# Optimization experiments

Hardware: AMD Instinct MI355X
Metric: run time of the kernel (lower is better)

## Reference

```python
import jax, jax.numpy as jnp
import numpy as np

H = W = 56; WS = 7; SHIFT = 3; HEADS = 4; DIM = 128
HD = DIM // HEADS; SCALE = HD ** -0.5
NW = (H // WS) * (W // WS)  # 64 windows per image
N = WS * WS                 # 49 tokens per window
HID = int(DIM * 4.0)


def _rel_index():
    coords = np.stack(np.meshgrid(np.arange(WS), np.arange(WS), indexing='ij'))  # (2,WS,WS)
    cf = coords.reshape(2, -1)
    rel = (cf[:, :, None] - cf[:, None, :]).transpose(1, 2, 0)  # (N,N,2)
    rel[:, :, 0] += WS - 1
    rel[:, :, 1] += WS - 1
    rel[:, :, 0] *= 2 * WS - 1
    return jnp.asarray(rel.sum(-1))  # (N,N) int indices into bias table


def _attn_mask():
    img = np.zeros((H, W))
    cnt = 0
    for hs in (slice(0, -WS), slice(-WS, -SHIFT), slice(-SHIFT, None)):
        for ws in (slice(0, -WS), slice(-WS, -SHIFT), slice(-SHIFT, None)):
            img[hs, ws] = cnt
            cnt += 1
    mw = img.reshape(H // WS, WS, W // WS, WS).transpose(0, 2, 1, 3).reshape(-1, N)
    diff = mw[:, None, :] - mw[:, :, None]
    return jnp.asarray(np.where(diff != 0, -100.0, 0.0).astype(np.float32))  # (NW,N,N)

REL_IDX = _rel_index()
ATTN_MASK = _attn_mask()


def _ln(x, g, b):
    m = jnp.mean(x, -1, keepdims=True)
    v = jnp.var(x, -1, keepdims=True)
    return (x - m) * jax.lax.rsqrt(v + 1e-5) * g + b


def _win_part(x):  # (B,H,W,C) -> (B*NW, N, C)
    B = x.shape[0]
    x = x.reshape(B, H // WS, WS, W // WS, WS, DIM)
    return x.transpose(0, 1, 3, 2, 4, 5).reshape(-1, N, DIM)


def _win_rev(x, B):  # (B*NW, N, C) -> (B,H,W,C)
    x = x.reshape(B, H // WS, W // WS, WS, WS, DIM)
    return x.transpose(0, 1, 3, 2, 4, 5).reshape(B, H, W, DIM)


def setup_inputs() -> dict:
    key = jax.random.key(0)
    ks = jax.random.split(key, 8)
    s = 0.02
    return {
        'x': jax.random.normal(ks[0], (64, H * W, DIM), jnp.float32),
        'g1': jnp.ones((DIM,), jnp.float32),
        'b1': jnp.zeros((DIM,), jnp.float32),
        'qkv_w': jax.random.normal(ks[1], (3 * DIM, DIM), jnp.float32) * s,
        'qkv_b': jnp.zeros((3 * DIM,), jnp.float32),
        'rpb_table': jax.random.normal(ks[2], ((2 * WS - 1) ** 2, HEADS), jnp.float32) * s,
        'proj_w': jax.random.normal(ks[3], (DIM, DIM), jnp.float32) * s,
        'proj_b': jnp.zeros((DIM,), jnp.float32),
        'g2': jnp.ones((DIM,), jnp.float32),
        'b2': jnp.zeros((DIM,), jnp.float32),
        'fc1_w': jax.random.normal(ks[4], (HID, DIM), jnp.float32) * s,
        'fc1_b': jnp.zeros((HID,), jnp.float32),
        'fc2_w': jax.random.normal(ks[5], (DIM, HID), jnp.float32) * s,
        'fc2_b': jnp.zeros((DIM,), jnp.float32),
    }


def reference(x, g1, b1, qkv_w, qkv_b, rpb_table, proj_w, proj_b, g2, b2, fc1_w, fc1_b, fc2_w, fc2_b):
    B = x.shape[0]
    shortcut = x
    h = _ln(x, g1, b1).reshape(B, H, W, DIM)
    # cyclic shift + window partition
    h = jnp.roll(h, shift=(-SHIFT, -SHIFT), axis=(1, 2))
    xw = _win_part(h)  # (B*NW, N, C)
    B_ = xw.shape[0]
    # window attention
    qkv = (xw @ qkv_w.T + qkv_b).reshape(B_, N, 3, HEADS, HD).transpose(2, 0, 3, 1, 4)
    q, k, v = qkv[0] * SCALE, qkv[1], qkv[2]  # (B_, heads, N, hd)
    attn = jnp.einsum('bhnd,bhmd->bhnm', q, k)
    bias = rpb_table[REL_IDX.reshape(-1)].reshape(N, N, HEADS).transpose(2, 0, 1)  # (heads,N,N)
    attn = attn + bias[None]
    attn = attn.reshape(B, NW, HEADS, N, N) + ATTN_MASK[None, :, None]
    attn = jax.nn.softmax(attn.reshape(B_, HEADS, N, N), axis=-1)
    out = jnp.einsum('bhnm,bhmd->bhnd', attn, v).transpose(0, 2, 1, 3).reshape(B_, N, DIM)
    out = out @ proj_w.T + proj_b
    # reverse windows + reverse shift
    h = _win_rev(out, B)
    h = jnp.roll(h, shift=(SHIFT, SHIFT), axis=(1, 2)).reshape(B, H * W, DIM)
    x = shortcut + h
    # MLP
    y = _ln(x, g2, b2)
    y = jax.nn.gelu(y @ fc1_w.T + fc1_b, approximate=False)
    y = y @ fc2_w.T + fc2_b
    return x + y
```

## Files before the change

### kernel.cpp

```cpp
#include <hip/hip_runtime.h>

typedef unsigned int uint;
typedef unsigned short ushort;
using short8 = __attribute__((ext_vector_type(8))) short;
using f32x4  = __attribute__((ext_vector_type(4))) float;
using uint4v = __attribute__((ext_vector_type(4))) uint;

#define SCALE_ 0.17677669529663687f
#define MFMA(a,b,c) __builtin_amdgcn_mfma_f32_16x16x32_bf16(a,b,c,0,0,0)

__device__ inline ushort f2bf(float f){
  uint u = __float_as_uint(f);
  return (ushort)((u + 0x7fffu + ((u >> 16) & 1u)) >> 16);
}
__device__ inline uint pk2(float a, float b){
  return (uint)f2bf(a) | ((uint)f2bf(b) << 16);
}
__device__ inline float gelu(float v){
  return 0.5f * v * (1.f + erff(v * 0.70710678f));
}

__global__ __launch_bounds__(256) void prep_kernel(
    const float* __restrict__ qkv_w, const float* __restrict__ qkv_b,
    const float* __restrict__ rpb, const float* __restrict__ proj_w,
    const float* __restrict__ fc1_w, const float* __restrict__ fc2_w,
    ushort* __restrict__ qkv_wb, float* __restrict__ qkv_bs,
    ushort* __restrict__ proj_wb, ushort* __restrict__ fc1_wb,
    ushort* __restrict__ fc2_wb, float* __restrict__ T2)
{
  int i = blockIdx.x * 256 + threadIdx.x;
  if (i < 49152) qkv_wb[i] = f2bf(qkv_w[i] * (i < 16384 ? SCALE_ : 1.f));
  if (i < 16384) proj_wb[i] = f2bf(proj_w[i]);
  if (i < 65536) { fc1_wb[i] = f2bf(fc1_w[i]); fc2_wb[i] = f2bf(fc2_w[i]); }
  if (i < 384)   qkv_bs[i] = qkv_b[i] * (i < 128 ? SCALE_ : 1.f);
  if (i < 65536) {
    int cls = i >> 14, h = (i >> 12) & 3, tok = (i >> 6) & 63, key = i & 63;
    float val = -30000.f;
    if (tok < 49 && key < 49) {
      int ri = tok / 7, ci = tok - ri * 7, rj = key / 7, cj = key - rj * 7;
      val = rpb[((ri - rj + 6) * 13 + (ci - cj + 6)) * 4 + h];
      int er = cls >> 1, ec = cls & 1;
      int regi = (er ? (ri < 4 ? 1 : 2) : 0) * 3 + (ec ? (ci < 4 ? 1 : 2) : 0);
      int regj = (er ? (rj < 4 ? 1 : 2) : 0) * 3 + (ec ? (cj < 4 ? 1 : 2) : 0);
      if (regi != regj) val -= 100.f;
    }
    T2[i] = val;
  }
}

__global__ __launch_bounds__(256, 3) void attn_kernel(
    const float* __restrict__ x, const float* __restrict__ g1, const float* __restrict__ b1,
    const ushort* __restrict__ qkv_wb, const float* __restrict__ qkv_bs,
    const float* __restrict__ T2, const ushort* __restrict__ proj_wb,
    const float* __restrict__ proj_b, float* __restrict__ x_new)
{
  __shared__ __align__(16) char smem[49152];
  const int tid = threadIdx.x;
  const int w = tid >> 6, lane = tid & 63;
  const int g = lane >> 4, li = lane & 15;
  const int blk = blockIdx.x;
  const int b = blk >> 6, wi = blk & 63;
  const int wr = wi >> 3, wc = wi & 7;
  const float* xb = x + (size_t)b * (3136 * 128);
  char* qls = smem + w * 4096;
  char* kls = smem + 16384 + w * 4096;
  char* vls = smem + 32768 + w * 4096;
  char* xls = smem + 32768;
  ushort* oa = (ushort*)smem;
  float* Rp = (float*)(smem + 17408);
  const f32x4 zf = {0.f, 0.f, 0.f, 0.f};

#pragma unroll
  for (int it = 0; it < 7; ++it) {
    int gi = it * 256 + tid;
    bool ok = gi < 1568;
    int t = ok ? (gi >> 5) : 48;
    int ch4 = (gi & 31) << 2;
    int tr = t / 7, tc = t - tr * 7;
    int rr = wr * 7 + tr + 3; rr -= (rr >= 56) ? 56 : 0;
    int cc = wc * 7 + tc + 3; cc -= (cc >= 56) ? 56 : 0;
    float4 v = *(const float4*)(xb + (size_t)(rr * 56 + cc) * 128 + ch4);
    float s = v.x + v.y + v.z + v.w;
    float s2 = v.x*v.x + v.y*v.y + v.z*v.z + v.w*v.w;
#pragma unroll
    for (int off = 16; off; off >>= 1) { s += __shfl_xor(s, off); s2 += __shfl_xor(s2, off); }
    float mn = s * 0.0078125f;
    float rs = rsqrtf(s2 * 0.0078125f - mn * mn + 1e-5f);
    if (ok) {
      float4 gg = *(const float4*)(g1 + ch4);
      float4 bb = *(const float4*)(b1 + ch4);
      uint2 u;
      u.x = pk2((v.x - mn) * rs * gg.x + bb.x, (v.y - mn) * rs * gg.y + bb.y);
      u.y = pk2((v.z - mn) * rs * gg.z + bb.z, (v.w - mn) * rs * gg.w + bb.w);
      int slot = ch4 >> 3;
      int tokx = t ^ ((slot & 7) << 1);
      *(uint2*)(xls + (slot * 64 + tokx) * 16 + ((ch4 & 4) << 1)) = u;
    }
  }
  if (tid < 240) {
    int slot = tid & 15, t = 49 + (tid >> 4);
    int tokx = t ^ ((slot & 7) << 1);
    uint4 z = make_uint4(0u, 0u, 0u, 0u);
    *(uint4*)(xls + (slot * 64 + tokx) * 16) = z;
  }
  __syncthreads();

  f32x4 qacc[2][4], kacc[2][4], vacc[4][2];
#pragma unroll
  for (int cf = 0; cf < 2; ++cf)
#pragma unroll
    for (int m = 0; m < 4; ++m) { qacc[cf][m] = zf; kacc[cf][m] = zf; vacc[m][cf] = zf; }

#pragma unroll
  for (int kt = 0; kt < 4; ++kt) {
    const int slot = kt * 4 + g;
    short8 xf[4];
#pragma unroll
    for (int m = 0; m < 4; ++m)
      xf[m] = *(const short8*)(xls + (slot * 64 + ((m * 16 + li) ^ ((slot & 7) << 1))) * 16);
    const int wofs = kt * 32 + g * 8;
#pragma unroll
    for (int cf = 0; cf < 2; ++cf) {
      short8 wq = *(const short8*)(qkv_wb + (size_t)(w * 32 + cf * 16 + li) * 128 + wofs);
#pragma unroll
      for (int m = 0; m < 4; ++m) qacc[cf][m] = MFMA(wq, xf[m], qacc[cf][m]);
    }
#pragma unroll
    for (int cf = 0; cf < 2; ++cf) {
      short8 wk = *(const short8*)(qkv_wb + (size_t)(128 + w * 32 + cf * 16 + li) * 128 + wofs);
#pragma unroll
      for (int m = 0; m < 4; ++m) kacc[cf][m] = MFMA(wk, xf[m], kacc[cf][m]);
    }
#pragma unroll
    for (int cf = 0; cf < 2; ++cf) {
      short8 wv = *(const short8*)(qkv_wb + (size_t)(256 + w * 32 + cf * 16 + li) * 128 + wofs);
#pragma unroll
      for (int m = 0; m < 4; ++m) vacc[m][cf] = MFMA(xf[m], wv, vacc[m][cf]);
    }
  }
#pragma unroll
  for (int cf = 0; cf < 2; ++cf) {
    f32x4 qb4 = *(const f32x4*)(qkv_bs + w * 32 + cf * 16 + g * 4);
    f32x4 kb4 = *(const f32x4*)(qkv_bs + 128 + w * 32 + cf * 16 + g * 4);
    const int qkoff = (cf * 2 + (g >> 1)) * 1024 + (g & 1) * 8;
#pragma unroll
    for (int m = 0; m < 4; ++m) {
      f32x4 qv = qacc[cf][m] + qb4;
      uint2 qu; qu.x = pk2(qv[0], qv[1]); qu.y = pk2(qv[2], qv[3]);
      *(uint2*)(qls + qkoff + (m * 16 + li) * 16) = qu;
      f32x4 kv = kacc[cf][m] + kb4;
      uint2 ku; ku.x = pk2(kv[0], kv[1]); ku.y = pk2(kv[2], kv[3]);
      *(uint2*)(kls + qkoff + (m * 16 + li) * 16) = ku;
    }
  }
  __syncthreads();
#pragma unroll
  for (int cf = 0; cf < 2; ++cf) {
    float vb = qkv_bs[256 + w * 32 + cf * 16 + li];
#pragma unroll
    for (int m = 0; m < 4; ++m) {
      f32x4 vv = vacc[m][cf];
      uint2 vu; vu.x = pk2(vv[0] + vb, vv[1] + vb); vu.y = pk2(vv[2] + vb, vv[3] + vb);
      *(uint2*)(vls + (m * 2 + (g >> 1)) * 1024 + (cf * 16 + li) * 16 + (g & 1) * 8) = vu;
    }
  }

  f32x4 oacc[2][4];
  {
    const int cls = ((wr == 7) ? 2 : 0) | ((wc == 7) ? 1 : 0);
    const float* Tb = T2 + ((cls * 4 + w) << 12);
    short8 kf[4];
#pragma unroll
    for (int n = 0; n < 4; ++n)
      kf[n] = *(const short8*)(kls + g * 1024 + (n * 16 + li) * 16);
    uint up[4][4][2];
#pragma unroll
    for (int m = 0; m < 4; ++m) {
      short8 qf = *(const short8*)(qls + g * 1024 + (m * 16 + li) * 16);
      f32x4 s[4];
#pragma unroll
      for (int n = 0; n < 4; ++n) {
        s[n] = MFMA(kf[n], qf, zf);
        s[n] += *(const f32x4*)(Tb + (m * 16 + li) * 64 + n * 16 + g * 4);
      }
      float mx = -3.4e38f;
#pragma unroll
      for (int n = 0; n < 4; ++n)
        mx = fmaxf(mx, fmaxf(fmaxf(s[n][0], s[n][1]), fmaxf(s[n][2], s[n][3])));
      mx = fmaxf(mx, __shfl_xor(mx, 16));
      mx = fmaxf(mx, __shfl_xor(mx, 32));
      float sum = 0.f;
#pragma unroll
      for (int n = 0; n < 4; ++n)
#pragma unroll
        for (int r = 0; r < 4; ++r) { float e = __expf(s[n][r] - mx); s[n][r] = e; sum += e; }
      sum += __shfl_xor(sum, 16); sum += __shfl_xor(sum, 32);
      float rsm = 1.f / sum;
#pragma unroll
      for (int n = 0; n < 4; ++n) {
        up[m][n][0] = pk2(s[n][0] * rsm, s[n][1] * rsm);
        up[m][n][1] = pk2(s[n][2] * rsm, s[n][3] * rsm);
      }
    }
#pragma unroll
    for (int cf = 0; cf < 2; ++cf)
#pragma unroll
      for (int m = 0; m < 4; ++m) oacc[cf][m] = zf;
    const int srcA = ((g & 1) << 5) + li;
    const int hi = g >> 1;
#pragma unroll
    for (int kt = 0; kt < 2; ++kt) {
      short8 vt0 = *(const short8*)(vls + (kt * 4 + g) * 1024 + li * 16);
      short8 vt1 = *(const short8*)(vls + (kt * 4 + g) * 1024 + (16 + li) * 16);
#pragma unroll
      for (int m = 0; m < 4; ++m) {
        uint t00 = __shfl(up[m][kt * 2][0], srcA),      t10 = __shfl(up[m][kt * 2 + 1][0], srcA);
        uint t01 = __shfl(up[m][kt * 2][1], srcA),      t11 = __shfl(up[m][kt * 2 + 1][1], srcA);
        uint t02 = __shfl(up[m][kt * 2][0], srcA + 16), t12 = __shfl(up[m][kt * 2 + 1][0], srcA + 16);
        uint t03 = __shfl(up[m][kt * 2][1], srcA + 16), t13 = __shfl(up[m][kt * 2 + 1][1], srcA + 16);
        uint4v pu = { hi ? t10 : t00, hi ? t11 : t01, hi ? t12 : t02, hi ? t13 : t03 };
        short8 pf = __builtin_bit_cast(short8, pu);
        oacc[0][m] = MFMA(vt0, pf, oacc[0][m]);
        oacc[1][m] = MFMA(vt1, pf, oacc[1][m]);
      }
    }
  }
  __syncthreads();
#pragma unroll
  for (int cf = 0; cf < 2; ++cf)
#pragma unroll
    for (int m = 0; m < 4; ++m) {
      uint2 ou; ou.x = pk2(oacc[cf][m][0], oacc[cf][m][1]);
      ou.y = pk2(oacc[cf][m][2], oacc[cf][m][3]);
      *(uint2*)((char*)oa + ((m * 16 + li) * 136 + w * 32 + cf * 16 + g * 4) * 2) = ou;
    }
  __syncthreads();

  {
    f32x4 pacc[2][4];
#pragma unroll
    for (int cf = 0; cf < 2; ++cf)
#pragma unroll
      for (int m = 0; m < 4; ++m) pacc[cf][m] = zf;
#pragma unroll
    for (int kt = 0; kt < 4; ++kt) {
      short8 af[4];
#pragma unroll
      for (int m = 0; m < 4; ++m)
        af[m] = *(const short8*)((char*)oa + (m * 16 + li) * 272 + kt * 64 + g * 16);
#pragma unroll
      for (int cf = 0; cf < 2; ++cf) {
        short8 wp = *(const short8*)(proj_wb + (size_t)(w * 32 + cf * 16 + li) * 128 + kt * 32 + g * 8);
#pragma unroll
        for (int m = 0; m < 4; ++m) pacc[cf][m] = MFMA(af[m], wp, pacc[cf][m]);
      }
    }
#pragma unroll
    for (int cf = 0; cf < 2; ++cf) {
      int col = w * 32 + cf * 16 + li;
      float pb = proj_b[col];
#pragma unroll
      for (int m = 0; m < 4; ++m)
#pragma unroll
        for (int r = 0; r < 4; ++r) {
          int t2 = m * 16 + g * 4 + r;
          if (t2 < 49)
            Rp[t2 * 128 + (col ^ ((t2 & 7) << 2))] = pacc[cf][m][r] + pb;
        }
    }
  }
  __syncthreads();

#pragma unroll
  for (int it = 0; it < 7; ++it) {
    int gi = it * 256 + tid;
    if (gi < 1568) {
      int t = gi >> 5, ch4 = (gi & 31) << 2;
      int tr = t / 7, tc = t - tr * 7;
      int rr = wr * 7 + tr + 3; rr -= (rr >= 56) ? 56 : 0;
      int cc = wc * 7 + tc + 3; cc -= (cc >= 56) ? 56 : 0;
      size_t off = ((size_t)b * 3136 + rr * 56 + cc) * 128 + ch4;
      f32x4 d = *(const f32x4*)&Rp[t * 128 + (ch4 ^ ((t & 7) << 2))];
      float4 xr = *(const float4*)(x + off);
      float4 ov;
      ov.x = xr.x + d[0]; ov.y = xr.y + d[1];
      ov.z = xr.z + d[2]; ov.w = xr.w + d[3];
      *(float4*)(x_new + off) = ov;
    }
  }
}

__global__ __launch_bounds__(256, 4) void mlp_kernel(
    float* __restrict__ xio,
    const float* __restrict__ g2, const float* __restrict__ b2,
    const ushort* __restrict__ w1, const float* __restrict__ fb1,
    const ushort* __restrict__ w2, const float* __restrict__ fb2)
{
  __shared__ __align__(16) char smem[32768];
  char* Axs = smem;
  char* hls = smem + 16384;
  float* Rp = (float*)smem;
  const int tid = threadIdx.x, lane = tid & 63, w = tid >> 6;
  const int g = lane >> 4, li = lane & 15;
  float* xw = xio + (size_t)blockIdx.x * 64 * 128;
  const f32x4 zf = {0.f, 0.f, 0.f, 0.f};

#pragma unroll
  for (int it = 0; it < 8; ++it) {
    int gi = it * 256 + tid;
    int row = gi >> 5, ch4 = (gi & 31) << 2;
    float4 v = *(const float4*)(xw + row * 128 + ch4);
    float s = v.x + v.y + v.z + v.w;
    float s2 = v.x*v.x + v.y*v.y + v.z*v.z + v.w*v.w;
#pragma unroll
    for (int off = 16; off; off >>= 1) { s += __shfl_xor(s, off); s2 += __shfl_xor(s2, off); }
    float mn = s * 0.0078125f;
    float rs = rsqrtf(s2 * 0.0078125f - mn * mn + 1e-5f);
    float4 gg = *(const float4*)(g2 + ch4);
    float4 bb = *(const float4*)(b2 + ch4);
    uint2 u;
    u.x = pk2((v.x - mn) * rs * gg.x + bb.x, (v.y - mn) * rs * gg.y + bb.y);
    u.y = pk2((v.z - mn) * rs * gg.z + bb.z, (v.w - mn) * rs * gg.w + bb.w);
    int slot = ch4 >> 3;
    int tokx = row ^ ((slot & 7) << 1);
    *(uint2*)(Axs + (slot * 64 + tokx) * 16 + ((ch4 & 4) << 1)) = u;
  }
  __syncthreads();

  f32x4 acc2[4][2];
#pragma unroll
  for (int mi = 0; mi < 4; ++mi) { acc2[mi][0] = zf; acc2[mi][1] = zf; }

  for (int ck = 0; ck < 4; ++ck) {
    f32x4 acc1[2][4];
#pragma unroll
    for (int oi = 0; oi < 2; ++oi)
#pragma unroll
      for (int mi = 0; mi < 4; ++mi) acc1[oi][mi] = zf;
#pragma unroll
    for (int kt = 0; kt < 4; ++kt) {
      const int slot = kt * 4 + g;
      short8 xf[4];
#pragma unroll
      for (int mi = 0; mi < 4; ++mi)
        xf[mi] = *(const short8*)(Axs + (slot * 64 + ((mi * 16 + li) ^ ((slot & 7) << 1))) * 16);
#pragma unroll
      for (int oi = 0; oi < 2; ++oi) {
        short8 wf = *(const short8*)(w1 + (size_t)(ck * 128 + w * 32 + oi * 16 + li) * 128 + kt * 32 + g * 8);
#pragma unroll
        for (int mi = 0; mi < 4; ++mi) acc1[oi][mi] = MFMA(wf, xf[mi], acc1[oi][mi]);
      }
    }
#pragma unroll
    for (int oi = 0; oi < 2; ++oi) {
      f32x4 b4 = *(const f32x4*)(fb1 + ck * 128 + w * 32 + oi * 16 + g * 4);
#pragma unroll
      for (int mi = 0; mi < 4; ++mi) {
        f32x4 h = acc1[oi][mi] + b4;
        uint2 u; u.x = pk2(gelu(h[0]), gelu(h[1])); u.y = pk2(gelu(h[2]), gelu(h[3]));
        *(uint2*)(hls + ((w * 4 + oi * 2 + (g >> 1)) * 64 + mi * 16 + li) * 16 + ((g & 1) << 3)) = u;
      }
    }
    __syncthreads();
#pragma unroll
    for (int kt = 0; kt < 4; ++kt) {
      short8 hf[4];
#pragma unroll
      for (int mi = 0; mi < 4; ++mi)
        hf[mi] = *(const short8*)(hls + ((kt * 4 + g) * 64 + mi * 16 + li) * 16);
#pragma unroll
      for (int bo = 0; bo < 2; ++bo) {
        short8 wf = *(const short8*)(w2 + (size_t)(w * 32 + bo * 16 + li) * 512 + ck * 128 + kt * 32 + g * 8);
#pragma unroll
        for (int mi = 0; mi < 4; ++mi) acc2[mi][bo] = MFMA(hf[mi], wf, acc2[mi][bo]);
      }
    }
    __syncthreads();
  }

#pragma unroll
  for (int mi = 0; mi < 4; ++mi)
#pragma unroll
    for (int bo = 0; bo < 2; ++bo) {
      int out = w * 32 + bo * 16 + li;
#pragma unroll
      for (int r = 0; r < 4; ++r) {
        int tok = mi * 16 + g * 4 + r;
        Rp[tok * 128 + (out ^ ((tok & 7) << 2))] = acc2[mi][bo][r];
      }
    }
  __syncthreads();
#pragma unroll
  for (int it = 0; it < 8; ++it) {
    int gi = it * 256 + tid;
    int row = gi >> 5, ch4 = (gi & 31) << 2;
    f32x4 d = *(const f32x4*)&Rp[row * 128 + (ch4 ^ ((row & 7) << 2))];
    float4 xr = *(const float4*)(xw + row * 128 + ch4);
    float4 bb = *(const float4*)(fb2 + ch4);
    float4 ov;
    ov.x = xr.x + d[0] + bb.x; ov.y = xr.y + d[1] + bb.y;
    ov.z = xr.z + d[2] + bb.z; ov.w = xr.w + d[3] + bb.w;
    *(float4*)(xw + row * 128 + ch4) = ov;
  }
}

extern "C" void kernel_launch(void* const* d_in, const int* in_sizes, int n_in,
                              void* d_out, int out_size, void* d_ws, size_t ws_size,
                              hipStream_t stream)
{
  const float* x      = (const float*)d_in[0];
  const float* g1     = (const float*)d_in[1];
  const float* b1     = (const float*)d_in[2];
  const float* qkv_w  = (const float*)d_in[3];
  const float* qkv_b  = (const float*)d_in[4];
  const float* rpb    = (const float*)d_in[5];
  const float* proj_w = (const float*)d_in[6];
  const float* proj_b = (const float*)d_in[7];
  const float* g2     = (const float*)d_in[8];
  const float* b2     = (const float*)d_in[9];
  const float* fc1_w  = (const float*)d_in[10];
  const float* fc1_b  = (const float*)d_in[11];
  const float* fc2_w  = (const float*)d_in[12];
  const float* fc2_b  = (const float*)d_in[13];

  char* ws = (char*)d_ws;
  float*  T2      = (float*)ws;
  ushort* qkv_wb  = (ushort*)(ws + 262144);
  ushort* proj_wb = (ushort*)(ws + 360448);
  ushort* fc1_wb  = (ushort*)(ws + 393216);
  ushort* fc2_wb  = (ushort*)(ws + 524288);
  float*  qkv_bs  = (float*)(ws + 655360);
  float* out = (float*)d_out;

  prep_kernel<<<256, 256, 0, stream>>>(qkv_w, qkv_b, rpb, proj_w, fc1_w, fc2_w,
                                       qkv_wb, qkv_bs, proj_wb, fc1_wb, fc2_wb, T2);
  attn_kernel<<<4096, 256, 0, stream>>>(x, g1, b1, qkv_wb, qkv_bs, T2,
                                        proj_wb, proj_b, out);
  mlp_kernel<<<3136, 256, 0, stream>>>(out, g2, b2, fc1_wb, fc1_b, fc2_wb, fc2_b);
}
```

Before: 356.9 us.

## Fuse window attention and MLP into a single per-window kernel

Merges the attention kernel and the MLP kernel so each block processes one shifted window end to end. The residual result stays in registers and LDS instead of being written to global memory and re-read. The MLP now runs on 49-token windows padded to 64 rows, wasting about a quarter of its MFMA work. The fused kernel also keeps the attention kernel's launch bounds and larger LDS footprint, which can lower occupancy for the MLP phase and raise register pressure.

```diff
diff --git a/kernel.cpp b/kernel.cpp
--- a/kernel.cpp
+++ b/kernel.cpp
@@ -48,11 +48,15 @@
   }
 }
 
-__global__ __launch_bounds__(256, 3) void attn_kernel(
+__global__ __launch_bounds__(256, 3) void fused_kernel(
     const float* __restrict__ x, const float* __restrict__ g1, const float* __restrict__ b1,
     const ushort* __restrict__ qkv_wb, const float* __restrict__ qkv_bs,
     const float* __restrict__ T2, const ushort* __restrict__ proj_wb,
-    const float* __restrict__ proj_b, float* __restrict__ x_new)
+    const float* __restrict__ proj_b,
+    const float* __restrict__ g2, const float* __restrict__ b2,
+    const ushort* __restrict__ w1, const float* __restrict__ fb1,
+    const ushort* __restrict__ w2, const float* __restrict__ fb2,
+    float* __restrict__ out)
 {
   __shared__ __align__(16) char smem[49152];
   const int tid = threadIdx.x;
@@ -68,6 +72,9 @@
   char* xls = smem + 32768;
   ushort* oa = (ushort*)smem;
   float* Rp = (float*)(smem + 17408);
+  char* Axs = smem;
+  char* hls = smem + 16384;
+  float* Rp2 = (float*)smem;
   const f32x4 zf = {0.f, 0.f, 0.f, 0.f};
 
 #pragma unroll
@@ -271,59 +278,39 @@
   }
   __syncthreads();
 
-#pragma unroll
-  for (int it = 0; it < 7; ++it) {
-    int gi = it * 256 + tid;
-    if (gi < 1568) {
-      int t = gi >> 5, ch4 = (gi & 31) << 2;
-      int tr = t / 7, tc = t - tr * 7;
-      int rr = wr * 7 + tr + 3; rr -= (rr >= 56) ? 56 : 0;
-      int cc = wc * 7 + tc + 3; cc -= (cc >= 56) ? 56 : 0;
-      size_t off = ((size_t)b * 3136 + rr * 56 + cc) * 128 + ch4;
-      f32x4 d = *(const f32x4*)&Rp[t * 128 + (ch4 ^ ((t & 7) << 2))];
-      float4 xr = *(const float4*)(x + off);
-      float4 ov;
-      ov.x = xr.x + d[0]; ov.y = xr.y + d[1];
-      ov.z = xr.z + d[2]; ov.w = xr.w + d[3];
-      *(float4*)(x_new + off) = ov;
-    }
-  }
-}
-
-__global__ __launch_bounds__(256, 4) void mlp_kernel(
-    float* __restrict__ xio,
-    const float* __restrict__ g2, const float* __restrict__ b2,
-    const ushort* __restrict__ w1, const float* __restrict__ fb1,
-    const ushort* __restrict__ w2, const float* __restrict__ fb2)
-{
-  __shared__ __align__(16) char smem[32768];
-  char* Axs = smem;
-  char* hls = smem + 16384;
-  float* Rp = (float*)smem;
-  const int tid = threadIdx.x, lane = tid & 63, w = tid >> 6;
-  const int g = lane >> 4, li = lane & 15;
-  float* xw = xio + (size_t)blockIdx.x * 64 * 128;
-  const f32x4 zf = {0.f, 0.f, 0.f, 0.f};
-
-#pragma unroll
-  for (int it = 0; it < 8; ++it) {
-    int gi = it * 256 + tid;
-    int row = gi >> 5, ch4 = (gi & 31) << 2;
-    float4 v = *(const float4*)(xw + row * 128 + ch4);
-    float s = v.x + v.y + v.z + v.w;
-    float s2 = v.x*v.x + v.y*v.y + v.z*v.z + v.w*v.w;
-#pragma unroll
-    for (int off = 16; off; off >>= 1) { s += __shfl_xor(s, off); s2 += __shfl_xor(s2, off); }
-    float mn = s * 0.0078125f;
-    float rs = rsqrtf(s2 * 0.0078125f - mn * mn + 1e-5f);
+  float4 xn[8];
+  {
+    const int ch4 = (lane & 31) << 2;
+    const int half = lane >> 5;
+    const int row0 = w * 16;
     float4 gg = *(const float4*)(g2 + ch4);
     float4 bb = *(const float4*)(b2 + ch4);
-    uint2 u;
-    u.x = pk2((v.x - mn) * rs * gg.x + bb.x, (v.y - mn) * rs * gg.y + bb.y);
-    u.y = pk2((v.z - mn) * rs * gg.z + bb.z, (v.w - mn) * rs * gg.w + bb.w);
-    int slot = ch4 >> 3;
-    int tokx = row ^ ((slot & 7) << 1);
-    *(uint2*)(Axs + (slot * 64 + tokx) * 16 + ((ch4 & 4) << 1)) = u;
+#pragma unroll
+    for (int it = 0; it < 8; ++it) {
+      int t = row0 + it * 2 + half;
+      float4 v = make_float4(0.f, 0.f, 0.f, 0.f);
+      if (t < 49) {
+        int tr = t / 7, tc = t - tr * 7;
+        int rr = wr * 7 + tr + 3; rr -= (rr >= 56) ? 56 : 0;
+        int cc = wc * 7 + tc + 3; cc -= (cc >= 56) ? 56 : 0;
+        float4 xr = *(const float4*)(xb + (size_t)(rr * 56 + cc) * 128 + ch4);
+        f32x4 d = *(const f32x4*)&Rp[t * 128 + (ch4 ^ ((t & 7) << 2))];
+        v.x = xr.x + d[0]; v.y = xr.y + d[1]; v.z = xr.z + d[2]; v.w = xr.w + d[3];
+      }
+      xn[it] = v;
+      float s = v.x + v.y + v.z + v.w;
+      float s2 = v.x*v.x + v.y*v.y + v.z*v.z + v.w*v.w;
+#pragma unroll
+      for (int off = 16; off; off >>= 1) { s += __shfl_xor(s, off); s2 += __shfl_xor(s2, off); }
+      float mn = s * 0.0078125f;
+      float rs = rsqrtf(s2 * 0.0078125f - mn * mn + 1e-5f);
+      uint2 u;
+      u.x = pk2((v.x - mn) * rs * gg.x + bb.x, (v.y - mn) * rs * gg.y + bb.y);
+      u.y = pk2((v.z - mn) * rs * gg.z + bb.z, (v.w - mn) * rs * gg.w + bb.w);
+      int slot = ch4 >> 3;
+      int tokx = t ^ ((slot & 7) << 1);
+      *(uint2*)(Axs + (slot * 64 + tokx) * 16 + ((ch4 & 4) << 1)) = u;
+    }
   }
   __syncthreads();
 
@@ -382,25 +369,35 @@
   for (int mi = 0; mi < 4; ++mi)
 #pragma unroll
     for (int bo = 0; bo < 2; ++bo) {
-      int out = w * 32 + bo * 16 + li;
+      int och = w * 32 + bo * 16 + li;
 #pragma unroll
       for (int r = 0; r < 4; ++r) {
         int tok = mi * 16 + g * 4 + r;
-        Rp[tok * 128 + (out ^ ((tok & 7) << 2))] = acc2[mi][bo][r];
-      }
-    }
-  __syncthreads();
-#pragma unroll
-  for (int it = 0; it < 8; ++it) {
-    int gi = it * 256 + tid;
-    int row = gi >> 5, ch4 = (gi & 31) << 2;
-    f32x4 d = *(const f32x4*)&Rp[row * 128 + (ch4 ^ ((row & 7) << 2))];
-    float4 xr = *(const float4*)(xw + row * 128 + ch4);
-    float4 bb = *(const float4*)(fb2 + ch4);
-    float4 ov;
-    ov.x = xr.x + d[0] + bb.x; ov.y = xr.y + d[1] + bb.y;
-    ov.z = xr.z + d[2] + bb.z; ov.w = xr.w + d[3] + bb.w;
-    *(float4*)(xw + row * 128 + ch4) = ov;
+        Rp2[tok * 128 + (och ^ ((tok & 7) << 2))] = acc2[mi][bo][r];
+      }
+    }
+  __syncthreads();
+  {
+    const int ch4 = (lane & 31) << 2;
+    const int half = lane >> 5;
+    const int row0 = w * 16;
+    float4 fb4 = *(const float4*)(fb2 + ch4);
+    float* ob = out + (size_t)b * (3136 * 128);
+#pragma unroll
+    for (int it = 0; it < 8; ++it) {
+      int t = row0 + it * 2 + half;
+      if (t < 49) {
+        int tr = t / 7, tc = t - tr * 7;
+        int rr = wr * 7 + tr + 3; rr -= (rr >= 56) ? 56 : 0;
+        int cc = wc * 7 + tc + 3; cc -= (cc >= 56) ? 56 : 0;
+        f32x4 d = *(const f32x4*)&Rp2[t * 128 + (ch4 ^ ((t & 7) << 2))];
+        float4 v = xn[it];
+        float4 ov;
+        ov.x = v.x + d[0] + fb4.x; ov.y = v.y + d[1] + fb4.y;
+        ov.z = v.z + d[2] + fb4.z; ov.w = v.w + d[3] + fb4.w;
+        *(float4*)(ob + (size_t)(rr * 56 + cc) * 128 + ch4) = ov;
+      }
+    }
   }
 }
 
@@ -434,7 +431,7 @@
 
   prep_kernel<<<256, 256, 0, stream>>>(qkv_w, qkv_b, rpb, proj_w, fc1_w, fc2_w,
                                        qkv_wb, qkv_bs, proj_wb, fc1_wb, fc2_wb, T2);
-  attn_kernel<<<4096, 256, 0, stream>>>(x, g1, b1, qkv_wb, qkv_bs, T2,
-                                        proj_wb, proj_b, out);
-  mlp_kernel<<<3136, 256, 0, stream>>>(out, g2, b2, fc1_wb, fc1_b, fc2_wb, fc2_b);
-}
+  fused_kernel<<<4096, 256, 0, stream>>>(x, g1, b1, qkv_wb, qkv_bs, T2,
+                                         proj_wb, proj_b, g2, b2,
+                                         fc1_wb, fc1_b, fc2_wb, fc2_b, out);
+}
```

After: 468.4 us. 31.3% more time.

## Keep Q/K/V in registers via lane shuffles, shrink LDS for more occupancy

Applied to the files above, without the earlier changes.

Q, K and V are now computed one after another, packed to bf16 and kept in registers. Operand fragments for the QK^T and PV MFMAs are rebuilt with cross-lane shuffles instead of being staged through LDS, which removes the QKV LDS buffers and one barrier. Shared memory drops from 48KB to about 25KB, with the x, attention-output and projection buffers aliased on one region (an extra barrier guards the reuse), and launch bounds rise to 4 blocks per CU. The cost is many more shuffle instructions and higher register pressure under the tighter launch bound, which may cause spills.

```diff
diff --git a/kernel.cpp b/kernel.cpp
--- a/kernel.cpp
+++ b/kernel.cpp
@@ -48,13 +48,16 @@
   }
 }
 
-__global__ __launch_bounds__(256, 3) void attn_kernel(
+__global__ __launch_bounds__(256, 4) void attn_kernel(
     const float* __restrict__ x, const float* __restrict__ g1, const float* __restrict__ b1,
     const ushort* __restrict__ qkv_wb, const float* __restrict__ qkv_bs,
     const float* __restrict__ T2, const ushort* __restrict__ proj_wb,
     const float* __restrict__ proj_b, float* __restrict__ x_new)
 {
-  __shared__ __align__(16) char smem[49152];
+  __shared__ __align__(16) char smem[25088];
+  char*   xls = smem;
+  ushort* oa  = (ushort*)smem;
+  float*  Rp  = (float*)smem;
   const int tid = threadIdx.x;
   const int w = tid >> 6, lane = tid & 63;
   const int g = lane >> 4, li = lane & 15;
@@ -62,12 +65,6 @@
   const int b = blk >> 6, wi = blk & 63;
   const int wr = wi >> 3, wc = wi & 7;
   const float* xb = x + (size_t)b * (3136 * 128);
-  char* qls = smem + w * 4096;
-  char* kls = smem + 16384 + w * 4096;
-  char* vls = smem + 32768 + w * 4096;
-  char* xls = smem + 32768;
-  ushort* oa = (ushort*)smem;
-  float* Rp = (float*)(smem + 17408);
   const f32x4 zf = {0.f, 0.f, 0.f, 0.f};
 
 #pragma unroll
@@ -105,78 +102,126 @@
   }
   __syncthreads();
 
-  f32x4 qacc[2][4], kacc[2][4], vacc[4][2];
-#pragma unroll
-  for (int cf = 0; cf < 2; ++cf)
-#pragma unroll
-    for (int m = 0; m < 4; ++m) { qacc[cf][m] = zf; kacc[cf][m] = zf; vacc[m][cf] = zf; }
-
-#pragma unroll
-  for (int kt = 0; kt < 4; ++kt) {
-    const int slot = kt * 4 + g;
-    short8 xf[4];
-#pragma unroll
-    for (int m = 0; m < 4; ++m)
-      xf[m] = *(const short8*)(xls + (slot * 64 + ((m * 16 + li) ^ ((slot & 7) << 1))) * 16);
-    const int wofs = kt * 32 + g * 8;
+  uint2 qp[2][4], kp[2][4], vp[4][2];
+  {
+    f32x4 qacc[2][4];
+#pragma unroll
+    for (int cf = 0; cf < 2; ++cf)
+#pragma unroll
+      for (int m = 0; m < 4; ++m) qacc[cf][m] = zf;
+#pragma unroll
+    for (int kt = 0; kt < 4; ++kt) {
+      const int slot = kt * 4 + g;
+      short8 xf[4];
+#pragma unroll
+      for (int m = 0; m < 4; ++m)
+        xf[m] = *(const short8*)(xls + (slot * 64 + ((m * 16 + li) ^ ((slot & 7) << 1))) * 16);
+      const int wofs = kt * 32 + g * 8;
+#pragma unroll
+      for (int cf = 0; cf < 2; ++cf) {
+        short8 wq = *(const short8*)(qkv_wb + (size_t)(w * 32 + cf * 16 + li) * 128 + wofs);
+#pragma unroll
+        for (int m = 0; m < 4; ++m) qacc[cf][m] = MFMA(wq, xf[m], qacc[cf][m]);
+      }
+    }
 #pragma unroll
     for (int cf = 0; cf < 2; ++cf) {
-      short8 wq = *(const short8*)(qkv_wb + (size_t)(w * 32 + cf * 16 + li) * 128 + wofs);
-#pragma unroll
-      for (int m = 0; m < 4; ++m) qacc[cf][m] = MFMA(wq, xf[m], qacc[cf][m]);
+      f32x4 qb4 = *(const f32x4*)(qkv_bs + w * 32 + cf * 16 + g * 4);
+#pragma unroll
+      for (int m = 0; m < 4; ++m) {
+        f32x4 qv = qacc[cf][m] + qb4;
+        qp[cf][m].x = pk2(qv[0], qv[1]); qp[cf][m].y = pk2(qv[2], qv[3]);
+      }
+    }
+  }
+  {
+    f32x4 kacc[2][4];
+#pragma unroll
+    for (int cf = 0; cf < 2; ++cf)
+#pragma unroll
+      for (int m = 0; m < 4; ++m) kacc[cf][m] = zf;
+#pragma unroll
+    for (int kt = 0; kt < 4; ++kt) {
+      const int slot = kt * 4 + g;
+      short8 xf[4];
+#pragma unroll
+      for (int m = 0; m < 4; ++m)
+        xf[m] = *(const short8*)(xls + (slot * 64 + ((m * 16 + li) ^ ((slot & 7) << 1))) * 16);
+      const int wofs = kt * 32 + g * 8;
+#pragma unroll
+      for (int cf = 0; cf < 2; ++cf) {
+        short8 wk = *(const short8*)(qkv_wb + (size_t)(128 + w * 32 + cf * 16 + li) * 128 + wofs);
+#pragma unroll
+        for (int m = 0; m < 4; ++m) kacc[cf][m] = MFMA(wk, xf[m], kacc[cf][m]);
+      }
     }
 #pragma unroll
     for (int cf = 0; cf < 2; ++cf) {
-      short8 wk = *(const short8*)(qkv_wb + (size_t)(128 + w * 32 + cf * 16 + li) * 128 + wofs);
-#pragma unroll
-      for (int m = 0; m < 4; ++m) kacc[cf][m] = MFMA(wk, xf[m], kacc[cf][m]);
+      f32x4 kb4 = *(const f32x4*)(qkv_bs + 128 + w * 32 + cf * 16 + g * 4);
+#pragma unroll
+      for (int m = 0; m < 4; ++m) {
+        f32x4 kv = kacc[cf][m] + kb4;
+        kp[cf][m].x = pk2(kv[0], kv[1]); kp[cf][m].y = pk2(kv[2], kv[3]);
+      }
+    }
+  }
+  {
+    f32x4 vacc[4][2];
+#pragma unroll
+    for (int m = 0; m < 4; ++m) { vacc[m][0] = zf; vacc[m][1] = zf; }
+#pragma unroll
+    for (int kt = 0; kt < 4; ++kt) {
+      const int slot = kt * 4 + g;
+      short8 xf[4];
+#pragma unroll
+      for (int m = 0; m < 4; ++m)
+        xf[m] = *(const short8*)(xls + (slot * 64 + ((m * 16 + li) ^ ((slot & 7) << 1))) * 16);
+      const int wofs = kt * 32 + g * 8;
+#pragma unroll
+      for (int cf = 0; cf < 2; ++cf) {
+        short8 wv = *(const short8*)(qkv_wb + (size_t)(256 + w * 32 + cf * 16 + li) * 128 + wofs);
+#pragma unroll
+        for (int m = 0; m < 4; ++m) vacc[m][cf] = MFMA(xf[m], wv, vacc[m][cf]);
+      }
     }
 #pragma unroll
     for (int cf = 0; cf < 2; ++cf) {
-      short8 wv = *(const short8*)(qkv_wb + (size_t)(256 + w * 32 + cf * 16 + li) * 128 + wofs);
-#pragma unroll
-      for (int m = 0; m < 4; ++m) vacc[m][cf] = MFMA(xf[m], wv, vacc[m][cf]);
-    }
-  }
-#pragma unroll
-  for (int cf = 0; cf < 2; ++cf) {
-    f32x4 qb4 = *(const f32x4*)(qkv_bs + w * 32 + cf * 16 + g * 4);
-    f32x4 kb4 = *(const f32x4*)(qkv_bs + 128 + w * 32 + cf * 16 + g * 4);
-    const int qkoff = (cf * 2 + (g >> 1)) * 1024 + (g & 1) * 8;
-#pragma unroll
-    for (int m = 0; m < 4; ++m) {
-      f32x4 qv = qacc[cf][m] + qb4;
-      uint2 qu; qu.x = pk2(qv[0], qv[1]); qu.y = pk2(qv[2], qv[3]);
-      *(uint2*)(qls + qkoff + (m * 16 + li) * 16) = qu;
-      f32x4 kv = kacc[cf][m] + kb4;
-      uint2 ku; ku.x = pk2(kv[0], kv[1]); ku.y = pk2(kv[2], kv[3]);
-      *(uint2*)(kls + qkoff + (m * 16 + li) * 16) = ku;
-    }
-  }
-  __syncthreads();
-#pragma unroll
-  for (int cf = 0; cf < 2; ++cf) {
-    float vb = qkv_bs[256 + w * 32 + cf * 16 + li];
-#pragma unroll
-    for (int m = 0; m < 4; ++m) {
-      f32x4 vv = vacc[m][cf];
-      uint2 vu; vu.x = pk2(vv[0] + vb, vv[1] + vb); vu.y = pk2(vv[2] + vb, vv[3] + vb);
-      *(uint2*)(vls + (m * 2 + (g >> 1)) * 1024 + (cf * 16 + li) * 16 + (g & 1) * 8) = vu;
+      float vb = qkv_bs[256 + w * 32 + cf * 16 + li];
+#pragma unroll
+      for (int m = 0; m < 4; ++m) {
+        f32x4 vv = vacc[m][cf];
+        vp[m][cf].x = pk2(vv[0] + vb, vv[1] + vb);
+        vp[m][cf].y = pk2(vv[2] + vb, vv[3] + vb);
+      }
     }
   }
 
   f32x4 oacc[2][4];
   {
+    const int srcA = ((g & 1) << 5) + li;
+    const int srcB = srcA + 16;
+    const int hi = g >> 1;
     const int cls = ((wr == 7) ? 2 : 0) | ((wc == 7) ? 1 : 0);
     const float* Tb = T2 + ((cls * 4 + w) << 12);
     short8 kf[4];
 #pragma unroll
-    for (int n = 0; n < 4; ++n)
-      kf[n] = *(const short8*)(kls + g * 1024 + (n * 16 + li) * 16);
+    for (int n = 0; n < 4; ++n) {
+      uint a0 = __shfl(kp[0][n].x, srcA), a1 = __shfl(kp[0][n].y, srcA);
+      uint a2 = __shfl(kp[0][n].x, srcB), a3 = __shfl(kp[0][n].y, srcB);
+      uint b0 = __shfl(kp[1][n].x, srcA), b1 = __shfl(kp[1][n].y, srcA);
+      uint b2 = __shfl(kp[1][n].x, srcB), b3 = __shfl(kp[1][n].y, srcB);
+      uint4v u = { hi ? b0 : a0, hi ? b1 : a1, hi ? b2 : a2, hi ? b3 : a3 };
+      kf[n] = __builtin_bit_cast(short8, u);
+    }
     uint up[4][4][2];
 #pragma unroll
     for (int m = 0; m < 4; ++m) {
-      short8 qf = *(const short8*)(qls + g * 1024 + (m * 16 + li) * 16);
+      uint a0 = __shfl(qp[0][m].x, srcA), a1 = __shfl(qp[0][m].y, srcA);
+      uint a2 = __shfl(qp[0][m].x, srcB), a3 = __shfl(qp[0][m].y, srcB);
+      uint b0 = __shfl(qp[1][m].x, srcA), b1 = __shfl(qp[1][m].y, srcA);
+      uint b2 = __shfl(qp[1][m].x, srcB), b3 = __shfl(qp[1][m].y, srcB);
+      uint4v uq = { hi ? b0 : a0, hi ? b1 : a1, hi ? b2 : a2, hi ? b3 : a3 };
+      short8 qf = __builtin_bit_cast(short8, uq);
       f32x4 s[4];
 #pragma unroll
       for (int n = 0; n < 4; ++n) {
@@ -206,22 +251,28 @@
     for (int cf = 0; cf < 2; ++cf)
 #pragma unroll
       for (int m = 0; m < 4; ++m) oacc[cf][m] = zf;
-    const int srcA = ((g & 1) << 5) + li;
-    const int hi = g >> 1;
 #pragma unroll
     for (int kt = 0; kt < 2; ++kt) {
-      short8 vt0 = *(const short8*)(vls + (kt * 4 + g) * 1024 + li * 16);
-      short8 vt1 = *(const short8*)(vls + (kt * 4 + g) * 1024 + (16 + li) * 16);
+      short8 vt[2];
+#pragma unroll
+      for (int half = 0; half < 2; ++half) {
+        uint a0 = __shfl(vp[kt * 2][half].x, srcA), a1 = __shfl(vp[kt * 2][half].y, srcA);
+        uint a2 = __shfl(vp[kt * 2][half].x, srcB), a3 = __shfl(vp[kt * 2][half].y, srcB);
+        uint b0 = __shfl(vp[kt * 2 + 1][half].x, srcA), b1 = __shfl(vp[kt * 2 + 1][half].y, srcA);
+        uint b2 = __shfl(vp[kt * 2 + 1][half].x, srcB), b3 = __shfl(vp[kt * 2 + 1][half].y, srcB);
+        uint4v uv = { hi ? b0 : a0, hi ? b1 : a1, hi ? b2 : a2, hi ? b3 : a3 };
+        vt[half] = __builtin_bit_cast(short8, uv);
+      }
 #pragma unroll
       for (int m = 0; m < 4; ++m) {
-        uint t00 = __shfl(up[m][kt * 2][0], srcA),      t10 = __shfl(up[m][kt * 2 + 1][0], srcA);
-        uint t01 = __shfl(up[m][kt * 2][1], srcA),      t11 = __shfl(up[m][kt * 2 + 1][1], srcA);
-        uint t02 = __shfl(up[m][kt * 2][0], srcA + 16), t12 = __shfl(up[m][kt * 2 + 1][0], srcA + 16);
-        uint t03 = __shfl(up[m][kt * 2][1], srcA + 16), t13 = __shfl(up[m][kt * 2 + 1][1], srcA + 16);
+        uint t00 = __shfl(up[m][kt * 2][0], srcA),  t10 = __shfl(up[m][kt * 2 + 1][0], srcA);
+        uint t01 = __shfl(up[m][kt * 2][1], srcA),  t11 = __shfl(up[m][kt * 2 + 1][1], srcA);
+        uint t02 = __shfl(up[m][kt * 2][0], srcB),  t12 = __shfl(up[m][kt * 2 + 1][0], srcB);
+        uint t03 = __shfl(up[m][kt * 2][1], srcB),  t13 = __shfl(up[m][kt * 2 + 1][1], srcB);
         uint4v pu = { hi ? t10 : t00, hi ? t11 : t01, hi ? t12 : t02, hi ? t13 : t03 };
         short8 pf = __builtin_bit_cast(short8, pu);
-        oacc[0][m] = MFMA(vt0, pf, oacc[0][m]);
-        oacc[1][m] = MFMA(vt1, pf, oacc[1][m]);
+        oacc[0][m] = MFMA(vt[0], pf, oacc[0][m]);
+        oacc[1][m] = MFMA(vt[1], pf, oacc[1][m]);
       }
     }
   }
@@ -236,38 +287,37 @@
     }
   __syncthreads();
 
-  {
-    f32x4 pacc[2][4];
-#pragma unroll
-    for (int cf = 0; cf < 2; ++cf)
-#pragma unroll
-      for (int m = 0; m < 4; ++m) pacc[cf][m] = zf;
-#pragma unroll
-    for (int kt = 0; kt < 4; ++kt) {
-      short8 af[4];
-#pragma unroll
-      for (int m = 0; m < 4; ++m)
-        af[m] = *(const short8*)((char*)oa + (m * 16 + li) * 272 + kt * 64 + g * 16);
-#pragma unroll
-      for (int cf = 0; cf < 2; ++cf) {
-        short8 wp = *(const short8*)(proj_wb + (size_t)(w * 32 + cf * 16 + li) * 128 + kt * 32 + g * 8);
-#pragma unroll
-        for (int m = 0; m < 4; ++m) pacc[cf][m] = MFMA(af[m], wp, pacc[cf][m]);
-      }
-    }
+  f32x4 pacc[2][4];
+#pragma unroll
+  for (int cf = 0; cf < 2; ++cf)
+#pragma unroll
+    for (int m = 0; m < 4; ++m) pacc[cf][m] = zf;
+#pragma unroll
+  for (int kt = 0; kt < 4; ++kt) {
+    short8 af[4];
+#pragma unroll
+    for (int m = 0; m < 4; ++m)
+      af[m] = *(const short8*)((char*)oa + (m * 16 + li) * 272 + kt * 64 + g * 16);
 #pragma unroll
     for (int cf = 0; cf < 2; ++cf) {
-      int col = w * 32 + cf * 16 + li;
-      float pb = proj_b[col];
-#pragma unroll
-      for (int m = 0; m < 4; ++m)
-#pragma unroll
-        for (int r = 0; r < 4; ++r) {
-          int t2 = m * 16 + g * 4 + r;
-          if (t2 < 49)
-            Rp[t2 * 128 + (col ^ ((t2 & 7) << 2))] = pacc[cf][m][r] + pb;
-        }
-    }
+      short8 wp = *(const short8*)(proj_wb + (size_t)(w * 32 + cf * 16 + li) * 128 + kt * 32 + g * 8);
+#pragma unroll
+      for (int m = 0; m < 4; ++m) pacc[cf][m] = MFMA(af[m], wp, pacc[cf][m]);
+    }
+  }
+  __syncthreads();
+#pragma unroll
+  for (int cf = 0; cf < 2; ++cf) {
+    int col = w * 32 + cf * 16 + li;
+    float pb = proj_b[col];
+#pragma unroll
+    for (int m = 0; m < 4; ++m)
+#pragma unroll
+      for (int r = 0; r < 4; ++r) {
+        int t2 = m * 16 + g * 4 + r;
+        if (t2 < 49)
+          Rp[t2 * 128 + (col ^ ((t2 & 7) << 2))] = pacc[cf][m][r] + pb;
+      }
   }
   __syncthreads();
 
```

Result: slower. 423.5 us (+18.7%).
